# Kernel tuning notes

Hardware: AMD Instinct MI355X
Metric: run time of the kernel (lower is better)

The kernel has to match this reference:

```python
import jax, jax.numpy as jnp
import numpy as np

T_MAX = 20
NUM_HEADS = 8
COMPLEXITY_W = 0.3
LN_EPS = 1e-5


def _layernorm(h, g, b):
    mu = jnp.mean(h, axis=-1, keepdims=True)
    var = jnp.var(h, axis=-1, keepdims=True)
    return (h - mu) / jnp.sqrt(var + LN_EPS) * g + b


def _gate_mlp(x, W1, b1, g, be, W2, b2, W3, b3):
    # Linear -> LayerNorm -> ReLU -> (Dropout=id in eval) -> Linear -> ReLU -> Linear -> Sigmoid
    h = jax.nn.relu(_layernorm(x @ W1 + b1, g, be))
    h = jax.nn.relu(h @ W2 + b2)
    return jax.nn.sigmoid(h @ W3 + b3)


def _adaptive_windows(x, p):
    S = x.shape[1]
    gate = _gate_mlp(x, p['gW1'], p['gb1'], p['gg'], p['gbe'], p['gW2'], p['gb2'], p['gW3'], p['gb3'])
    comp = _gate_mlp(x, p['cW1'], p['cb1'], p['cg'], p['cbe'], p['cW2'], p['cb2'], p['cW3'], p['cb3'])
    pos = jnp.linspace(0.8, 1.2, S, dtype=x.dtype).reshape(1, -1, 1)
    score = ((1.0 - COMPLEXITY_W) * gate + COMPLEXITY_W * comp) * pos
    T_i = jnp.clip(jnp.ceil(score[..., 0] * T_MAX), 1, T_MAX).astype(jnp.int32)  # [B,S]
    return T_i


def _spike_sum(x, T_i, alpha, beta):
    # LIF recurrence over T_MAX steps; accumulate masked spikes. x: [B,S,E]
    z = jnp.zeros_like(x)

    def step(carry, t):
        v, i, acc = carry
        active = (t < T_i).astype(x.dtype)[..., None]  # [B,S,1]
        i = alpha * i + x * active
        v = beta * v + i
        s = (v >= 1.0).astype(x.dtype)
        v = v * (1.0 - s)  # v_reset = 0
        return (v, i, acc + s * active), None

    (_, _, acc), _ = jax.lax.scan(step, (z, z, z), jnp.arange(T_MAX))
    return acc


def _forward(x, params):
    B, S, E = x.shape
    H, D = NUM_HEADS, E // NUM_HEADS
    q = x @ params['Wq']
    k = x @ params['Wk']
    v = x @ params['Wv']
    T_i = _adaptive_windows(x, params)
    q_sum = _spike_sum(q, T_i, params['alpha_q'], params['beta_q'])
    k_sum = _spike_sum(k, T_i, params['alpha_k'], params['beta_k'])
    v_mean = _spike_sum(v, T_i, params['alpha_v'], params['beta_v']) / T_MAX
    q_sum = q_sum.reshape(B, S, H, D)
    k_sum = k_sum.reshape(B, S, H, D)
    v_mean = v_mean.reshape(B, S, H, D)
    scale = D ** -0.5
    scores = jnp.einsum('bihd,bjhd->bhij', q_sum, k_sum) * scale
    w = jax.nn.softmax(scores, axis=-1)
    out = jnp.einsum('bhij,bjhd->bihd', w, v_mean).reshape(B, S, E)
    return out @ params['Wo'] + params['bo']


def setup_inputs() -> dict:
    key = jax.random.key(0)
    ks = iter(jax.random.split(key, 32))
    B, S, E = 4, 1024, 512
    f32 = jnp.float32

    def w(shape, scale=0.02):
        return jax.random.normal(next(ks), shape, dtype=f32) * scale

    inp = {
        'x': jax.random.normal(next(ks), (B, S, E), dtype=f32),
        'Wq': w((E, E)), 'Wk': w((E, E)), 'Wv': w((E, E)),
        'Wo': w((E, E)), 'bo': jnp.zeros((E,), f32),
        'gW1': w((E, 128)), 'gb1': jnp.zeros((128,), f32),
        'gg': jnp.ones((128,), f32), 'gbe': jnp.zeros((128,), f32),
        'gW2': w((128, 64)), 'gb2': jnp.zeros((64,), f32),
        'gW3': w((64, 1)), 'gb3': jnp.zeros((1,), f32),
        'cW1': w((E, 64)), 'cb1': jnp.zeros((64,), f32),
        'cg': jnp.ones((64,), f32), 'cbe': jnp.zeros((64,), f32),
        'cW2': w((64, 32)), 'cb2': jnp.zeros((32,), f32),
        'cW3': w((32, 1)), 'cb3': jnp.zeros((1,), f32),
        'alpha_q': jnp.asarray(np.exp(-1 / 5.0), f32), 'beta_q': jnp.asarray(np.exp(-1 / 20.0), f32),
        'alpha_k': jnp.asarray(np.exp(-1 / 5.0), f32), 'beta_k': jnp.asarray(np.exp(-1 / 20.0), f32),
        'alpha_v': jnp.asarray(np.exp(-1 / 5.0), f32), 'beta_v': jnp.asarray(np.exp(-1 / 20.0), f32),
    }
    return inp


def reference(x, Wq, Wk, Wv, Wo, bo,
              gW1, gb1, gg, gbe, gW2, gb2, gW3, gb3,
              cW1, cb1, cg, cbe, cW2, cb2, cW3, cb3,
              alpha_q, beta_q, alpha_k, beta_k, alpha_v, beta_v):
    params = dict(Wq=Wq, Wk=Wk, Wv=Wv, Wo=Wo, bo=bo,
                  gW1=gW1, gb1=gb1, gg=gg, gbe=gbe, gW2=gW2, gb2=gb2, gW3=gW3, gb3=gb3,
                  cW1=cW1, cb1=cb1, cg=cg, cbe=cbe, cW2=cW2, cb2=cb2, cW3=cW3, cb3=cb3,
                  alpha_q=alpha_q, beta_q=beta_q, alpha_k=alpha_k, beta_k=beta_k,
                  alpha_v=alpha_v, beta_v=beta_v)
    return _forward(x, params)
```

## Files before the change

kernel.cpp:

```cpp
#include <hip/hip_runtime.h>
#include <math.h>

#define SEQ   1024
#define EMB   512
#define NROWS 4096
#define LDP   72
#define GROWS 4

typedef __attribute__((ext_vector_type(8))) short short8;
typedef __attribute__((ext_vector_type(4))) float float4v;

__device__ __forceinline__ float bf2f(unsigned short s) {
    union { float f; unsigned u; } x; x.u = ((unsigned)s) << 16; return x.f;
}
__device__ __forceinline__ unsigned short f2bf(float f) {
    union { float f; unsigned u; } x; x.f = f;
    unsigned r = x.u + 0x7fffu + ((x.u >> 16) & 1u);
    return (unsigned short)(r >> 16);
}

__device__ __forceinline__ void gld16(const unsigned short* g, short* l) {
    __builtin_amdgcn_global_load_lds(
        (__attribute__((address_space(1))) void*)(g),
        (__attribute__((address_space(3))) void*)(l), 16, 0, 0);
}

__device__ __forceinline__ void split3(float x, unsigned short& h, unsigned short& m, unsigned short& l) {
    union { float f; unsigned u; } a; a.f = x;
    const unsigned rh = a.u + 0x7fffu + ((a.u >> 16) & 1u);
    h = (unsigned short)(rh >> 16);
    union { float f; unsigned u; } hf; hf.u = rh & 0xffff0000u;
    const float r1 = x - hf.f;
    a.f = r1;
    const unsigned rm = a.u + 0x7fffu + ((a.u >> 16) & 1u);
    m = (unsigned short)(rm >> 16);
    union { float f; unsigned u; } mf; mf.u = rm & 0xffff0000u;
    const float r2 = r1 - mf.f;
    l = f2bf(r2);
}

template<int H1, int H2>
__device__ __forceinline__ double mlp_eval(
    const double xs[GROWS][EMB], double* h1, double* h2, double* red,
    double* mu_s, double* var_s,
    const float* __restrict__ W1, const float* __restrict__ b1,
    const float* __restrict__ gam, const float* __restrict__ bet,
    const float* __restrict__ W2, const float* __restrict__ b2,
    const float* __restrict__ W3, const float* __restrict__ b3,
    int tid, int myrow)
{
    constexpr int S  = 256 / H1;
    constexpr int KS = EMB / S;

    {
        const int col = tid % H1, sk = tid / H1;
        double acc[GROWS] = {0.0, 0.0, 0.0, 0.0};
        const int kbeg = sk * KS;
        #pragma unroll 4
        for (int k = kbeg; k < kbeg + KS; ++k) {
            const double w = (double)W1[k * H1 + col];
            #pragma unroll
            for (int r = 0; r < GROWS; ++r) acc[r] += w * xs[r][k];
        }
        #pragma unroll
        for (int r = 0; r < GROWS; ++r) red[(sk * GROWS + r) * H1 + col] = acc[r];
    }
    __syncthreads();
    for (int idx = tid; idx < GROWS * H1; idx += 256) {
        const int r = idx / H1, cc = idx % H1;
        double s = 0.0;
        #pragma unroll
        for (int t = 0; t < S; ++t) s += red[(t * GROWS + r) * H1 + cc];
        h1[r * H1 + cc] = s + (double)b1[cc];
    }
    __syncthreads();

    {
        const int w = tid >> 6, l = tid & 63;
        double s = 0.0;
        for (int c = l; c < H1; c += 64) s += h1[w * H1 + c];
        #pragma unroll
        for (int off = 32; off >= 1; off >>= 1) s += __shfl_xor(s, off);
        if (l == 0) mu_s[w] = s / (double)H1;
    }
    __syncthreads();
    {
        const int w = tid >> 6, l = tid & 63;
        const double mu = mu_s[w];
        double s = 0.0;
        for (int c = l; c < H1; c += 64) { const double d = h1[w * H1 + c] - mu; s += d * d; }
        #pragma unroll
        for (int off = 32; off >= 1; off >>= 1) s += __shfl_xor(s, off);
        if (l == 0) var_s[w] = s / (double)H1;
    }
    __syncthreads();
    for (int idx = tid; idx < GROWS * H1; idx += 256) {
        const int r = idx / H1, cc = idx % H1;
        double hn = (h1[r * H1 + cc] - mu_s[r]) / sqrt(var_s[r] + 1e-5) * (double)gam[cc] + (double)bet[cc];
        h1[r * H1 + cc] = hn > 0.0 ? hn : 0.0;
    }
    __syncthreads();

    {
        const int col = tid % H2;
        const int r   = tid / H2;
        if (r < GROWS) {
            double acc = (double)b2[col];
            for (int k = 0; k < H1; ++k)
                acc += (double)W2[k * H2 + col] * h1[r * H1 + k];
            h2[r * H2 + col] = acc > 0.0 ? acc : 0.0;
        }
    }
    __syncthreads();

    {
        const int w = tid >> 6, l = tid & 63;
        double s = 0.0;
        for (int c = l; c < H2; c += 64) s += h2[w * H2 + c] * (double)W3[c];
        #pragma unroll
        for (int off = 32; off >= 1; off >>= 1) s += __shfl_xor(s, off);
        if (l == 0) mu_s[w] = s;
    }
    __syncthreads();
    double ret = 0.0;
    if (myrow >= 0) {
        const double z = mu_s[myrow] + (double)b3[0];
        ret = 1.0 / (1.0 + exp(-z));
    }
    return ret;
}

__global__ __launch_bounds__(256) void pre_kernel(
    const float* __restrict__ x,
    const float* __restrict__ gW1, const float* __restrict__ gb1,
    const float* __restrict__ gg,  const float* __restrict__ gbe,
    const float* __restrict__ gW2, const float* __restrict__ gb2,
    const float* __restrict__ gW3, const float* __restrict__ gb3,
    const float* __restrict__ cW1, const float* __restrict__ cb1,
    const float* __restrict__ cg,  const float* __restrict__ cbe,
    const float* __restrict__ cW2, const float* __restrict__ cb2,
    const float* __restrict__ cW3, const float* __restrict__ cb3,
    double* __restrict__ scores,
    const float* __restrict__ Wq, const float* __restrict__ Wk,
    const float* __restrict__ Wv, unsigned short* __restrict__ WL,
    unsigned short* __restrict__ XL,
    const float* __restrict__ Wo, unsigned short* __restrict__ WoT)
{
    __shared__ __align__(16) char smem[30784];
    const int bid = blockIdx.x;
    const int tid = threadIdx.x;

    if (bid < 2048) {
        double (*xs)[EMB] = (double(*)[EMB])smem;
        double* h1    = (double*)(smem + 16384);
        double* h2    = (double*)(smem + 20480);
        double* red   = (double*)(smem + 22528);
        double* mu_s  = (double*)(smem + 30720);
        double* var_s = (double*)(smem + 30752);

        const int gx = bid & 1023, gy = bid >> 10;
        const int row0 = gx * GROWS;

        for (int idx = tid; idx < GROWS * EMB; idx += 256) {
            const int r = idx >> 9, cc = idx & 511;
            xs[r][cc] = (double)x[(size_t)(row0 + r) * EMB + cc];
        }
        __syncthreads();

        const int myrow = (tid < GROWS) ? tid : -1;
        double v;
        if (gy == 0)
            v = mlp_eval<128, 64>(xs, h1, h2, red, mu_s, var_s,
                                  gW1, gb1, gg, gbe, gW2, gb2, gW3, gb3, tid, myrow);
        else
            v = mlp_eval<64, 32>(xs, h1, h2, red, mu_s, var_s,
                                 cW1, cb1, cg, cbe, cW2, cb2, cW3, cb3, tid, myrow);

        if (myrow >= 0)
            scores[(size_t)gy * NROWS + row0 + myrow] = v;

    } else if (bid < 3072) {
        unsigned short* Xh = XL;
        unsigned short* Xm = XL + (size_t)NROWS * EMB;
        unsigned short* Xl = Xm + (size_t)NROWS * EMB;
        const size_t i0 = ((size_t)(bid - 2048) * 256 + tid) * 8;
        const float4 a0 = *(const float4*)&x[i0];
        const float4 a1 = *(const float4*)&x[i0 + 4];
        const float av8[8] = {a0.x, a0.y, a0.z, a0.w, a1.x, a1.y, a1.z, a1.w};
        short8 ph, pm, pl;
        #pragma unroll
        for (int e = 0; e < 8; ++e) {
            unsigned short h, m, l;
            split3(av8[e], h, m, l);
            ph[e] = (short)h; pm[e] = (short)m; pl[e] = (short)l;
        }
        *(short8*)&Xh[i0] = ph;
        *(short8*)&Xm[i0] = pm;
        *(short8*)&Xl[i0] = pl;

    } else if (bid < 3264) {
        const int t = bid - 3072;
        const int z = t >> 6, rem = t & 63;
        const int k0 = (rem >> 3) * 64, n0 = (rem & 7) * 64;
        const float* __restrict__ W = (z == 0) ? Wq : (z == 1) ? Wk : Wv;
        unsigned short* Th = WL + (size_t)z * 3 * EMB * EMB;
        unsigned short* Tm = Th + (size_t)EMB * EMB;
        unsigned short* Tl = Tm + (size_t)EMB * EMB;

        float (*Ws)[68] = (float(*)[68])smem;
        #pragma unroll
        for (int it = 0; it < 4; ++it) {
            const int idx = it * 256 + tid;
            const int r = idx >> 4, c4 = (idx & 15) * 4;
            *(float4*)&Ws[r][c4] = *(const float4*)&W[(size_t)(k0 + r) * EMB + n0 + c4];
        }
        __syncthreads();
        #pragma unroll
        for (int it = 0; it < 2; ++it) {
            const int idx = it * 256 + tid;
            const int n = idx >> 3, k8 = (idx & 7) * 8;
            short8 ph, pm, pl;
            #pragma unroll
            for (int j = 0; j < 8; ++j) {
                unsigned short h, m, l;
                split3(Ws[k8 + j][n], h, m, l);
                ph[j] = (short)h; pm[j] = (short)m; pl[j] = (short)l;
            }
            const size_t o = (size_t)(n0 + n) * EMB + k0 + k8;
            *(short8*)&Th[o] = ph;
            *(short8*)&Tm[o] = pm;
            *(short8*)&Tl[o] = pl;
        }

    } else {
        const int t = bid - 3264;
        const int k0 = (t >> 3) * 64, n0 = (t & 7) * 64;
        unsigned short (*Ws)[72] = (unsigned short(*)[72])smem;
        #pragma unroll
        for (int it = 0; it < 4; ++it) {
            const int idx = it * 256 + tid;
            const int r = idx >> 4, c4 = (idx & 15) * 4;
            const float4 w4 = *(const float4*)&Wo[(size_t)(k0 + r) * EMB + n0 + c4];
            Ws[r][c4 + 0] = f2bf(w4.x); Ws[r][c4 + 1] = f2bf(w4.y);
            Ws[r][c4 + 2] = f2bf(w4.z); Ws[r][c4 + 3] = f2bf(w4.w);
        }
        __syncthreads();
        #pragma unroll
        for (int it = 0; it < 2; ++it) {
            const int idx = it * 256 + tid;
            const int n = idx >> 3, k8 = (idx & 7) * 8;
            short8 pack;
            #pragma unroll
            for (int j = 0; j < 8; ++j) pack[j] = (short)Ws[k8 + j][n];
            *(short8*)&WoT[(size_t)(n0 + n) * EMB + k0 + k8] = pack;
        }
    }
}

__global__ __launch_bounds__(256) void qkv_mfma_lif_kernel(
    const unsigned short* __restrict__ XL, const unsigned short* __restrict__ WL,
    const float* __restrict__ aq, const float* __restrict__ bq,
    const float* __restrict__ akp, const float* __restrict__ bkp,
    const float* __restrict__ av, const float* __restrict__ bv,
    const double* __restrict__ scores,
    unsigned short* __restrict__ q_sum, unsigned short* __restrict__ k_sum,
    unsigned short* __restrict__ v_mean)
{
    const int z = blockIdx.z;
    const unsigned short* __restrict__ WTh = WL + (size_t)z * 3 * EMB * EMB;
    const unsigned short* __restrict__ WTm = WTh + (size_t)EMB * EMB;
    const unsigned short* __restrict__ WTl = WTm + (size_t)EMB * EMB;
    const unsigned short* __restrict__ Xh = XL;
    const unsigned short* __restrict__ Xm = XL + (size_t)NROWS * EMB;
    const unsigned short* __restrict__ Xl = Xm + (size_t)NROWS * EMB;
    unsigned short* __restrict__ out = (z == 0) ? q_sum : (z == 1) ? k_sum : v_mean;
    const double alpha = (double)((z == 0) ? aq : (z == 1) ? akp : av)[0];
    const double beta  = (double)((z == 0) ? bq : (z == 1) ? bkp : bv)[0];

    const int phys = blockIdx.x + 8 * blockIdx.y;
    const int logical = (phys & 7) * 32 + (phys >> 3);
    const int bx = logical & 7, by = logical >> 3;
    const int row0 = by * 128, col0 = bx * 64;

    __shared__ __align__(16) short As[3][4096];
    __shared__ __align__(16) short Bs[3][2048];

    const int tid  = threadIdx.x;
    const int lane = tid & 63, wave = tid >> 6;
    const int qd = lane >> 4, c = lane & 15;
    const int wrow = wave * 32;

    const int kc8 = ((lane & 3) ^ ((lane >> 3) & 3)) * 8;
    const size_t ga0 = (size_t)(row0 + wave * 16 + (lane >> 2)) * EMB + kc8;
    const size_t ga1 = ga0 + (size_t)64 * EMB;
    const size_t gb  = (size_t)(col0 + wave * 16 + (lane >> 2)) * EMB + kc8;

    int arf[2], brf[4];
    #pragma unroll
    for (int i = 0; i < 2; ++i) {
        const int Ra = wrow + i * 16 + c;
        arf[i] = Ra * 32 + ((qd ^ ((Ra >> 1) & 3)) * 8);
    }
    #pragma unroll
    for (int j = 0; j < 4; ++j) {
        const int Rb = j * 16 + c;
        brf[j] = Rb * 32 + ((qd ^ ((Rb >> 1) & 3)) * 8);
    }

    float4v acc[2][4];
    #pragma unroll
    for (int i = 0; i < 2; ++i)
        #pragma unroll
        for (int j = 0; j < 4; ++j)
            acc[i][j] = (float4v){0.f, 0.f, 0.f, 0.f};

    for (int k0 = 0; k0 < EMB; k0 += 32) {
        __syncthreads();
        gld16(Xh  + ga0 + k0, &As[0][wave * 512]);
        gld16(Xh  + ga1 + k0, &As[0][2048 + wave * 512]);
        gld16(Xm  + ga0 + k0, &As[1][wave * 512]);
        gld16(Xm  + ga1 + k0, &As[1][2048 + wave * 512]);
        gld16(Xl  + ga0 + k0, &As[2][wave * 512]);
        gld16(Xl  + ga1 + k0, &As[2][2048 + wave * 512]);
        gld16(WTh + gb  + k0, &Bs[0][wave * 512]);
        gld16(WTm + gb  + k0, &Bs[1][wave * 512]);
        gld16(WTl + gb  + k0, &Bs[2][wave * 512]);
        __syncthreads();

        short8 Afh[2], Afm[2], Afl[2];
        #pragma unroll
        for (int i = 0; i < 2; ++i) {
            Afh[i] = *(const short8*)&As[0][arf[i]];
            Afm[i] = *(const short8*)&As[1][arf[i]];
            Afl[i] = *(const short8*)&As[2][arf[i]];
        }
        short8 Bfh[4], Bfm[4], Bfl[4];
        #pragma unroll
        for (int j = 0; j < 4; ++j) {
            Bfh[j] = *(const short8*)&Bs[0][brf[j]];
            Bfm[j] = *(const short8*)&Bs[1][brf[j]];
            Bfl[j] = *(const short8*)&Bs[2][brf[j]];
        }

        #pragma unroll
        for (int i = 0; i < 2; ++i)
            #pragma unroll
            for (int j = 0; j < 4; ++j) {
                float4v t = acc[i][j];
                t = __builtin_amdgcn_mfma_f32_16x16x32_bf16(Afh[i], Bfh[j], t, 0, 0, 0);
                t = __builtin_amdgcn_mfma_f32_16x16x32_bf16(Afh[i], Bfm[j], t, 0, 0, 0);
                t = __builtin_amdgcn_mfma_f32_16x16x32_bf16(Afm[i], Bfh[j], t, 0, 0, 0);
                t = __builtin_amdgcn_mfma_f32_16x16x32_bf16(Afm[i], Bfm[j], t, 0, 0, 0);
                t = __builtin_amdgcn_mfma_f32_16x16x32_bf16(Afh[i], Bfl[j], t, 0, 0, 0);
                t = __builtin_amdgcn_mfma_f32_16x16x32_bf16(Afl[i], Bfh[j], t, 0, 0, 0);
                acc[i][j] = t;
            }
    }

    #pragma unroll
    for (int i = 0; i < 2; ++i)
        #pragma unroll
        for (int r = 0; r < 4; ++r) {
            const int gm = row0 + wrow + i * 16 + qd * 4 + r;
            const double g0 = scores[gm];
            const double c0 = scores[NROWS + gm];
            const int s = gm & (SEQ - 1);
            const double step = (1.2 - 0.8) / (double)(SEQ - 1);
            const double pos  = (double)s * step + 0.8;
            const double score = ((1.0 - 0.3) * g0 + 0.3 * c0) * pos;
            double td = ceil(score * 20.0);
            td = td < 1.0 ? 1.0 : (td > 20.0 ? 20.0 : td);
            const int T = (int)td;
            double cur0 = 0.0, cur1 = 0.0, cur2 = 0.0, cur3 = 0.0;
            double vm0 = 0.0, vm1 = 0.0, vm2 = 0.0, vm3 = 0.0;
            double sp0 = 0.0, sp1 = 0.0, sp2 = 0.0, sp3 = 0.0;
            const double xv0 = (double)acc[i][0][r];
            const double xv1 = (double)acc[i][1][r];
            const double xv2 = (double)acc[i][2][r];
            const double xv3 = (double)acc[i][3][r];
            for (int t = 0; t < T; ++t) {
                cur0 = alpha * cur0 + xv0; vm0 = beta * vm0 + cur0;
                if (vm0 >= 1.0) { sp0 += 1.0; vm0 = 0.0; }
                cur1 = alpha * cur1 + xv1; vm1 = beta * vm1 + cur1;
                if (vm1 >= 1.0) { sp1 += 1.0; vm1 = 0.0; }
                cur2 = alpha * cur2 + xv2; vm2 = beta * vm2 + cur2;
                if (vm2 >= 1.0) { sp2 += 1.0; vm2 = 0.0; }
                cur3 = alpha * cur3 + xv3; vm3 = beta * vm3 + cur3;
                if (vm3 >= 1.0) { sp3 += 1.0; vm3 = 0.0; }
            }
            if (z == 2) { sp0 /= 20.0; sp1 /= 20.0; sp2 /= 20.0; sp3 /= 20.0; }
            const size_t ob = (size_t)gm * EMB + col0 + c;
            out[ob +  0] = f2bf((float)sp0);
            out[ob + 16] = f2bf((float)sp1);
            out[ob + 32] = f2bf((float)sp2);
            out[ob + 48] = f2bf((float)sp3);
        }
}

__global__ __launch_bounds__(256) void attn_mfma_kernel(
    const unsigned short* __restrict__ q, const unsigned short* __restrict__ k,
    const unsigned short* __restrict__ v, unsigned short* __restrict__ attn_bf)
{
    __shared__ __align__(16) short Ks[64 * LDP];
    __shared__ __align__(16) short Pt[64 * LDP];
    __shared__ __align__(16) short Vt[64 * LDP];

    const int b = blockIdx.z, h = blockIdx.y;
    const int i0 = blockIdx.x * 64;
    const int tid  = threadIdx.x;
    const int wave = tid >> 6, lane = tid & 63;
    const int quad = lane >> 4, c = lane & 15;

    const unsigned short* Qb = q + ((size_t)b * SEQ + i0) * EMB + h * 64;
    const unsigned short* Kb = k + (size_t)b * SEQ * EMB + h * 64;
    const unsigned short* Vb = v + (size_t)b * SEQ * EMB + h * 64;

    short8 qf[2];
    {
        const int qrow = wave * 16 + c;
        #pragma unroll
        for (int ks = 0; ks < 2; ++ks) {
            short8 raw = *(const short8*)(Qb + (size_t)qrow * EMB + ks * 32 + quad * 8);
            short8 sc8;
            #pragma unroll
            for (int j = 0; j < 8; ++j)
                sc8[j] = (short)f2bf(bf2f((unsigned short)raw[j]) * 0.125f);
            qf[ks] = sc8;
        }
    }

    float m_r[4], l_r[4];
    float4v o[4];
    #pragma unroll
    for (int r = 0; r < 4; ++r) { m_r[r] = -1e30f; l_r[r] = 0.f; }
    #pragma unroll
    for (int nb = 0; nb < 4; ++nb)
        #pragma unroll
        for (int r = 0; r < 4; ++r) o[nb][r] = 0.f;

    for (int jt = 0; jt < SEQ / 64; ++jt) {
        #pragma unroll
        for (int it = 0; it < 2; ++it) {
            const int idx = it * 256 + tid;
            const int row = idx >> 3, ch = idx & 7;
            short8 val = *(const short8*)(Kb + (size_t)(jt * 64 + row) * EMB + ch * 8);
            *(short8*)&Ks[row * LDP + ch * 8] = val;
        }
        __syncthreads();

        float sc[4][4];
        #pragma unroll
        for (int nb = 0; nb < 4; ++nb) {
            float4v acc = {0.f, 0.f, 0.f, 0.f};
            #pragma unroll
            for (int ks = 0; ks < 2; ++ks) {
                short8 bfrag = *(const short8*)&Ks[(nb * 16 + c) * LDP + ks * 32 + quad * 8];
                acc = __builtin_amdgcn_mfma_f32_16x16x32_bf16(qf[ks], bfrag, acc, 0, 0, 0);
            }
            #pragma unroll
            for (int r = 0; r < 4; ++r) sc[nb][r] = acc[r];
        }

        float mnew[4], alpha[4];
        #pragma unroll
        for (int r = 0; r < 4; ++r) {
            float mx = fmaxf(fmaxf(sc[0][r], sc[1][r]), fmaxf(sc[2][r], sc[3][r]));
            #pragma unroll
            for (int off = 8; off >= 1; off >>= 1) mx = fmaxf(mx, __shfl_xor(mx, off));
            mnew[r]  = fmaxf(m_r[r], mx);
            alpha[r] = __expf(m_r[r] - mnew[r]);
            m_r[r]   = mnew[r];
        }
        float psum[4] = {0.f, 0.f, 0.f, 0.f};
        #pragma unroll
        for (int nb = 0; nb < 4; ++nb)
            #pragma unroll
            for (int r = 0; r < 4; ++r) {
                float p = __expf(sc[nb][r] - mnew[r]);
                psum[r] += p;
                Pt[(wave * 16 + quad * 4 + r) * LDP + nb * 16 + c] = (short)f2bf(p);
            }
        #pragma unroll
        for (int r = 0; r < 4; ++r) {
            float s = psum[r];
            #pragma unroll
            for (int off = 8; off >= 1; off >>= 1) s += __shfl_xor(s, off);
            l_r[r] = l_r[r] * alpha[r] + s;
            #pragma unroll
            for (int nb = 0; nb < 4; ++nb) o[nb][r] *= alpha[r];
        }

        {
            const int m = tid & 7, rp = tid >> 3;
            const int r = rp * 2;
            short8 v0 = *(const short8*)(Vb + (size_t)(jt * 64 + r) * EMB + m * 8);
            short8 v1 = *(const short8*)(Vb + (size_t)(jt * 64 + r + 1) * EMB + m * 8);
            const int rch = r >> 3, rlow = r & 7;
            #pragma unroll
            for (int i = 0; i < 8; ++i) {
                const int d = m * 8 + i;
                const int col = ((rch ^ m) << 3) + rlow;
                *(int*)&Vt[d * LDP + col] =
                    (int)((unsigned)(unsigned short)v0[i] |
                          ((unsigned)(unsigned short)v1[i] << 16));
            }
        }
        __syncthreads();

        short8 pf[2];
        #pragma unroll
        for (int ks = 0; ks < 2; ++ks)
            pf[ks] = *(const short8*)&Pt[(wave * 16 + c) * LDP + ks * 32 + quad * 8];
        #pragma unroll
        for (int nb = 0; nb < 4; ++nb) {
            float4v acc = o[nb];
            #pragma unroll
            for (int ks = 0; ks < 2; ++ks) {
                const int d = nb * 16 + c;
                const int kch = ks * 4 + quad;
                const int col = ((kch ^ (d >> 3)) << 3);
                short8 vfrag = *(const short8*)&Vt[d * LDP + col];
                acc = __builtin_amdgcn_mfma_f32_16x16x32_bf16(pf[ks], vfrag, acc, 0, 0, 0);
            }
            o[nb] = acc;
        }
    }

    #pragma unroll
    for (int r = 0; r < 4; ++r) {
        const float inv = 1.0f / l_r[r];
        const int row = i0 + wave * 16 + quad * 4 + r;
        #pragma unroll
        for (int nb = 0; nb < 4; ++nb)
            attn_bf[((size_t)b * SEQ + row) * EMB + h * 64 + nb * 16 + c] =
                f2bf(o[nb][r] * inv);
    }
}

__global__ __launch_bounds__(256) void out_gemm_kernel(
    const unsigned short* __restrict__ A,
    const unsigned short* __restrict__ BT,
    const float* __restrict__ bias, float* __restrict__ out)
{
    __shared__ __align__(16) short Ao[2048], Bo[2048];

    const int tid  = threadIdx.x;
    const int lane = tid & 63, wave = tid >> 6;
    const int qd = lane >> 4, c = lane & 15;

    const int phys = blockIdx.x + 8 * blockIdx.y;
    const int logical = (phys & 7) * 64 + (phys >> 3);
    const int bx = logical & 7, by = logical >> 3;
    const int row0 = by * 64, col0 = bx * 64;

    const int kc8 = ((lane & 3) ^ ((lane >> 3) & 3)) * 8;
    const size_t ga = (size_t)(row0 + wave * 16 + (lane >> 2)) * EMB + kc8;
    const size_t gb = (size_t)(col0 + wave * 16 + (lane >> 2)) * EMB + kc8;

    int arf, brf[4];
    {
        const int Ra = wave * 16 + c;
        arf = Ra * 32 + ((qd ^ ((Ra >> 1) & 3)) * 8);
    }
    #pragma unroll
    for (int j = 0; j < 4; ++j) {
        const int Rb = j * 16 + c;
        brf[j] = Rb * 32 + ((qd ^ ((Rb >> 1) & 3)) * 8);
    }

    float4v acc[4];
    #pragma unroll
    for (int j = 0; j < 4; ++j) acc[j] = (float4v){0.f, 0.f, 0.f, 0.f};

    for (int k0 = 0; k0 < EMB; k0 += 32) {
        __syncthreads();
        gld16(A  + ga + k0, &Ao[wave * 512]);
        gld16(BT + gb + k0, &Bo[wave * 512]);
        __syncthreads();

        const short8 af = *(const short8*)&Ao[arf];
        #pragma unroll
        for (int j = 0; j < 4; ++j) {
            const short8 bf = *(const short8*)&Bo[brf[j]];
            acc[j] = __builtin_amdgcn_mfma_f32_16x16x32_bf16(af, bf, acc[j], 0, 0, 0);
        }
    }

    #pragma unroll
    for (int j = 0; j < 4; ++j)
        #pragma unroll
        for (int r = 0; r < 4; ++r) {
            const int gm = row0 + wave * 16 + qd * 4 + r;
            const int gn = col0 + j * 16 + c;
            out[(size_t)gm * EMB + gn] = acc[j][r] + bias[gn];
        }
}

extern "C" void kernel_launch(void* const* d_in, const int* in_sizes, int n_in,
                              void* d_out, int out_size, void* d_ws, size_t ws_size,
                              hipStream_t stream)
{
    const float* x   = (const float*)d_in[0];
    const float* Wq  = (const float*)d_in[1];
    const float* Wk  = (const float*)d_in[2];
    const float* Wv  = (const float*)d_in[3];
    const float* Wo  = (const float*)d_in[4];
    const float* bo  = (const float*)d_in[5];
    const float* gW1 = (const float*)d_in[6];
    const float* gb1 = (const float*)d_in[7];
    const float* gg  = (const float*)d_in[8];
    const float* gbe = (const float*)d_in[9];
    const float* gW2 = (const float*)d_in[10];
    const float* gb2 = (const float*)d_in[11];
    const float* gW3 = (const float*)d_in[12];
    const float* gb3 = (const float*)d_in[13];
    const float* cW1 = (const float*)d_in[14];
    const float* cb1 = (const float*)d_in[15];
    const float* cg  = (const float*)d_in[16];
    const float* cbe = (const float*)d_in[17];
    const float* cW2 = (const float*)d_in[18];
    const float* cb2 = (const float*)d_in[19];
    const float* cW3 = (const float*)d_in[20];
    const float* cb3 = (const float*)d_in[21];
    const float* aq  = (const float*)d_in[22];
    const float* bq  = (const float*)d_in[23];
    const float* ak  = (const float*)d_in[24];
    const float* bk  = (const float*)d_in[25];
    const float* av  = (const float*)d_in[26];
    const float* bv  = (const float*)d_in[27];

    unsigned short* q_sum   = (unsigned short*)((char*)d_ws + 16384);
    unsigned short* k_sum   = q_sum   + (size_t)NROWS * EMB;
    unsigned short* v_mean  = k_sum   + (size_t)NROWS * EMB;
    unsigned short* attn_bf = v_mean  + (size_t)NROWS * EMB;
    unsigned short* WoT     = attn_bf + (size_t)NROWS * EMB;
    unsigned short* WL      = WoT     + (size_t)EMB * EMB;
    unsigned short* XLp     = WL      + (size_t)9 * EMB * EMB;
    double* scores          = (double*)(XLp + (size_t)3 * NROWS * EMB);
    float* out = (float*)d_out;

    pre_kernel<<<dim3(3328), dim3(256), 0, stream>>>(
        x, gW1, gb1, gg, gbe, gW2, gb2, gW3, gb3,
        cW1, cb1, cg, cbe, cW2, cb2, cW3, cb3, scores,
        Wq, Wk, Wv, WL, XLp, Wo, WoT);

    qkv_mfma_lif_kernel<<<dim3(EMB / 64, NROWS / 128, 3), dim3(256), 0, stream>>>(
        XLp, WL, aq, bq, ak, bk, av, bv, scores, q_sum, k_sum, v_mean);

    attn_mfma_kernel<<<dim3(SEQ / 64, 8, 4), dim3(256), 0, stream>>>(
        q_sum, k_sum, v_mean, attn_bf);

    out_gemm_kernel<<<dim3(EMB / 64, NROWS / 64), dim3(256), 0, stream>>>(
        attn_bf, WoT, bo, out);
}
```

Before: 250.9 us.

## Double-buffer K/V tiles in attention and A/B tiles in output GEMM

The attention kernel now prefetches the next K and V tiles into registers while it computes the current tile, then stores them into a second LDS buffer. This removes one __syncthreads per iteration and hides global load latency. The output GEMM likewise switches from direct global-to-LDS loads with a K-step of 32 to register-prefetched, double-buffered 64-wide K tiles with a new XOR swizzle. The trade-off is more LDS and more registers per block, which may lower occupancy.

```diff
diff --git a/kernel.cpp b/kernel.cpp
--- a/kernel.cpp
+++ b/kernel.cpp
@@ -401,9 +401,9 @@
     const unsigned short* __restrict__ q, const unsigned short* __restrict__ k,
     const unsigned short* __restrict__ v, unsigned short* __restrict__ attn_bf)
 {
-    __shared__ __align__(16) short Ks[64 * LDP];
+    __shared__ __align__(16) short Ks2[2][64 * LDP];
+    __shared__ __align__(16) short Vt2[2][64 * LDP];
     __shared__ __align__(16) short Pt[64 * LDP];
-    __shared__ __align__(16) short Vt[64 * LDP];
 
     const int b = blockIdx.z, h = blockIdx.y;
     const int i0 = blockIdx.x * 64;
@@ -429,6 +429,29 @@
         }
     }
 
+    const int krow = tid >> 3, kch = tid & 7;
+    const int vm_  = tid & 7,  vrp = tid >> 3;
+    const int vr   = vrp * 2;
+    const int vrch = vr >> 3, vrlow = vr & 7;
+
+    short8 kr0, kr1, vv0, vv1;
+    kr0 = *(const short8*)(Kb + (size_t)krow * EMB + kch * 8);
+    kr1 = *(const short8*)(Kb + (size_t)(32 + krow) * EMB + kch * 8);
+    vv0 = *(const short8*)(Vb + (size_t)vr * EMB + vm_ * 8);
+    vv1 = *(const short8*)(Vb + (size_t)(vr + 1) * EMB + vm_ * 8);
+    {
+        *(short8*)&Ks2[0][krow * LDP + kch * 8] = kr0;
+        *(short8*)&Ks2[0][(32 + krow) * LDP + kch * 8] = kr1;
+        #pragma unroll
+        for (int i = 0; i < 8; ++i) {
+            const int d = vm_ * 8 + i;
+            const int col = ((vrch ^ vm_) << 3) + vrlow;
+            *(int*)&Vt2[0][d * LDP + col] =
+                (int)((unsigned)(unsigned short)vv0[i] |
+                      ((unsigned)(unsigned short)vv1[i] << 16));
+        }
+    }
+
     float m_r[4], l_r[4];
     float4v o[4];
     #pragma unroll
@@ -439,14 +462,17 @@
         for (int r = 0; r < 4; ++r) o[nb][r] = 0.f;
 
     for (int jt = 0; jt < SEQ / 64; ++jt) {
-        #pragma unroll
-        for (int it = 0; it < 2; ++it) {
-            const int idx = it * 256 + tid;
-            const int row = idx >> 3, ch = idx & 7;
-            short8 val = *(const short8*)(Kb + (size_t)(jt * 64 + row) * EMB + ch * 8);
-            *(short8*)&Ks[row * LDP + ch * 8] = val;
-        }
         __syncthreads();
+        const short* Ks = &Ks2[jt & 1][0];
+        const short* Vt = &Vt2[jt & 1][0];
+
+        if (jt + 1 < SEQ / 64) {
+            const size_t kb = (size_t)((jt + 1) * 64);
+            kr0 = *(const short8*)(Kb + (kb + krow) * EMB + kch * 8);
+            kr1 = *(const short8*)(Kb + (kb + 32 + krow) * EMB + kch * 8);
+            vv0 = *(const short8*)(Vb + (kb + vr) * EMB + vm_ * 8);
+            vv1 = *(const short8*)(Vb + (kb + vr + 1) * EMB + vm_ * 8);
+        }
 
         float sc[4][4];
         #pragma unroll
@@ -490,23 +516,6 @@
             for (int nb = 0; nb < 4; ++nb) o[nb][r] *= alpha[r];
         }
 
-        {
-            const int m = tid & 7, rp = tid >> 3;
-            const int r = rp * 2;
-            short8 v0 = *(const short8*)(Vb + (size_t)(jt * 64 + r) * EMB + m * 8);
-            short8 v1 = *(const short8*)(Vb + (size_t)(jt * 64 + r + 1) * EMB + m * 8);
-            const int rch = r >> 3, rlow = r & 7;
-            #pragma unroll
-            for (int i = 0; i < 8; ++i) {
-                const int d = m * 8 + i;
-                const int col = ((rch ^ m) << 3) + rlow;
-                *(int*)&Vt[d * LDP + col] =
-                    (int)((unsigned)(unsigned short)v0[i] |
-                          ((unsigned)(unsigned short)v1[i] << 16));
-            }
-        }
-        __syncthreads();
-
         short8 pf[2];
         #pragma unroll
         for (int ks = 0; ks < 2; ++ks)
@@ -517,12 +526,26 @@
             #pragma unroll
             for (int ks = 0; ks < 2; ++ks) {
                 const int d = nb * 16 + c;
-                const int kch = ks * 4 + quad;
-                const int col = ((kch ^ (d >> 3)) << 3);
+                const int kch2 = ks * 4 + quad;
+                const int col = ((kch2 ^ (d >> 3)) << 3);
                 short8 vfrag = *(const short8*)&Vt[d * LDP + col];
                 acc = __builtin_amdgcn_mfma_f32_16x16x32_bf16(pf[ks], vfrag, acc, 0, 0, 0);
             }
             o[nb] = acc;
+        }
+
+        if (jt + 1 < SEQ / 64) {
+            const int nb2 = (jt + 1) & 1;
+            *(short8*)&Ks2[nb2][krow * LDP + kch * 8] = kr0;
+            *(short8*)&Ks2[nb2][(32 + krow) * LDP + kch * 8] = kr1;
+            #pragma unroll
+            for (int i = 0; i < 8; ++i) {
+                const int d = vm_ * 8 + i;
+                const int col = ((vrch ^ vm_) << 3) + vrlow;
+                *(int*)&Vt2[nb2][d * LDP + col] =
+                    (int)((unsigned)(unsigned short)vv0[i] |
+                          ((unsigned)(unsigned short)vv1[i] << 16));
+            }
         }
     }
 
@@ -542,7 +565,7 @@
     const unsigned short* __restrict__ BT,
     const float* __restrict__ bias, float* __restrict__ out)
 {
-    __shared__ __align__(16) short Ao[2048], Bo[2048];
+    __shared__ __align__(16) short As2[2][4096], Bs2[2][4096];
 
     const int tid  = threadIdx.x;
     const int lane = tid & 63, wave = tid >> 6;
@@ -553,36 +576,52 @@
     const int bx = logical & 7, by = logical >> 3;
     const int row0 = by * 64, col0 = bx * 64;
 
-    const int kc8 = ((lane & 3) ^ ((lane >> 3) & 3)) * 8;
-    const size_t ga = (size_t)(row0 + wave * 16 + (lane >> 2)) * EMB + kc8;
-    const size_t gb = (size_t)(col0 + wave * 16 + (lane >> 2)) * EMB + kc8;
-
-    int arf, brf[4];
-    {
-        const int Ra = wave * 16 + c;
-        arf = Ra * 32 + ((qd ^ ((Ra >> 1) & 3)) * 8);
-    }
-    #pragma unroll
-    for (int j = 0; j < 4; ++j) {
-        const int Rb = j * 16 + c;
-        brf[j] = Rb * 32 + ((qd ^ ((Rb >> 1) & 3)) * 8);
+    const int sr = tid >> 2, sj = (tid & 3) * 2;
+    const size_t gA = (size_t)(row0 + sr) * EMB + sj * 8;
+    const size_t gB = (size_t)(col0 + sr) * EMB + sj * 8;
+    const int dA0 = sr * 64 + ((sj ^ (sr & 7)) * 8);
+    const int dA1 = sr * 64 + (((sj + 1) ^ (sr & 7)) * 8);
+
+    int arf[2], brf[4][2];
+    #pragma unroll
+    for (int kk = 0; kk < 2; ++kk) {
+        arf[kk] = (wave * 16 + c) * 64 + (((kk * 4 + qd) ^ (c & 7)) * 8);
+        #pragma unroll
+        for (int j = 0; j < 4; ++j)
+            brf[j][kk] = (j * 16 + c) * 64 + (((kk * 4 + qd) ^ (c & 7)) * 8);
     }
 
     float4v acc[4];
     #pragma unroll
     for (int j = 0; j < 4; ++j) acc[j] = (float4v){0.f, 0.f, 0.f, 0.f};
 
-    for (int k0 = 0; k0 < EMB; k0 += 32) {
+    short8 ra0, ra1, rb0, rb1;
+    ra0 = *(const short8*)&A[gA];      ra1 = *(const short8*)&A[gA + 8];
+    rb0 = *(const short8*)&BT[gB];     rb1 = *(const short8*)&BT[gB + 8];
+    *(short8*)&As2[0][dA0] = ra0; *(short8*)&As2[0][dA1] = ra1;
+    *(short8*)&Bs2[0][dA0] = rb0; *(short8*)&Bs2[0][dA1] = rb1;
+
+    for (int it = 0; it < 8; ++it) {
         __syncthreads();
-        gld16(A  + ga + k0, &Ao[wave * 512]);
-        gld16(BT + gb + k0, &Bo[wave * 512]);
-        __syncthreads();
-
-        const short8 af = *(const short8*)&Ao[arf];
-        #pragma unroll
-        for (int j = 0; j < 4; ++j) {
-            const short8 bf = *(const short8*)&Bo[brf[j]];
-            acc[j] = __builtin_amdgcn_mfma_f32_16x16x32_bf16(af, bf, acc[j], 0, 0, 0);
+        const int cur = it & 1;
+        if (it < 7) {
+            const int k0 = (it + 1) * 64;
+            ra0 = *(const short8*)&A[gA + k0];  ra1 = *(const short8*)&A[gA + k0 + 8];
+            rb0 = *(const short8*)&BT[gB + k0]; rb1 = *(const short8*)&BT[gB + k0 + 8];
+        }
+        #pragma unroll
+        for (int kk = 0; kk < 2; ++kk) {
+            const short8 af = *(const short8*)&As2[cur][arf[kk]];
+            #pragma unroll
+            for (int j = 0; j < 4; ++j) {
+                const short8 bf = *(const short8*)&Bs2[cur][brf[j][kk]];
+                acc[j] = __builtin_amdgcn_mfma_f32_16x16x32_bf16(af, bf, acc[j], 0, 0, 0);
+            }
+        }
+        if (it < 7) {
+            const int nxt = cur ^ 1;
+            *(short8*)&As2[nxt][dA0] = ra0; *(short8*)&As2[nxt][dA1] = ra1;
+            *(short8*)&Bs2[nxt][dA0] = rb0; *(short8*)&Bs2[nxt][dA1] = rb1;
         }
     }
 
```

After: 248.3 us, median of 2. Within noise of the previous version (-1.1%).

## Split attention KV range across two blocks with combine pass; double-buffer out GEMM

Applied to the files above, without the earlier changes.

The attention kernel now splits the key/value sequence into two halves and launches twice as many blocks. Each block writes unnormalized fp32 partial outputs plus its running max and sum to workspace, and a new combine kernel merges them flash-decoding style into bf16. This targets low occupancy on the attention launch (512 blocks on a large GPU), at the cost of extra fp32 traffic and an extra launch. Separately, the output GEMM moves to 64-wide K tiles with register-staged double buffering in swizzled LDS, halving the barriers and overlapping global loads with MFMA work.

```diff
diff --git a/kernel.cpp b/kernel.cpp
--- a/kernel.cpp
+++ b/kernel.cpp
@@ -399,13 +399,15 @@
 
 __global__ __launch_bounds__(256) void attn_mfma_kernel(
     const unsigned short* __restrict__ q, const unsigned short* __restrict__ k,
-    const unsigned short* __restrict__ v, unsigned short* __restrict__ attn_bf)
+    const unsigned short* __restrict__ v,
+    float* __restrict__ OP, float* __restrict__ MP, float* __restrict__ LP)
 {
     __shared__ __align__(16) short Ks[64 * LDP];
     __shared__ __align__(16) short Pt[64 * LDP];
     __shared__ __align__(16) short Vt[64 * LDP];
 
-    const int b = blockIdx.z, h = blockIdx.y;
+    const int b = blockIdx.z & 3, kv = blockIdx.z >> 2;
+    const int h = blockIdx.y;
     const int i0 = blockIdx.x * 64;
     const int tid  = threadIdx.x;
     const int wave = tid >> 6, lane = tid & 63;
@@ -438,7 +440,7 @@
         #pragma unroll
         for (int r = 0; r < 4; ++r) o[nb][r] = 0.f;
 
-    for (int jt = 0; jt < SEQ / 64; ++jt) {
+    for (int jt = kv * 8; jt < kv * 8 + 8; ++jt) {
         #pragma unroll
         for (int it = 0; it < 2; ++it) {
             const int idx = it * 256 + tid;
@@ -526,15 +528,43 @@
         }
     }
 
+    const size_t grb = (size_t)(b * 8 + h) * SEQ;
     #pragma unroll
     for (int r = 0; r < 4; ++r) {
-        const float inv = 1.0f / l_r[r];
         const int row = i0 + wave * 16 + quad * 4 + r;
+        const size_t gr = grb + row;
+        float* op = OP + (size_t)kv * 32768 * 64 + gr * 64;
         #pragma unroll
         for (int nb = 0; nb < 4; ++nb)
-            attn_bf[((size_t)b * SEQ + row) * EMB + h * 64 + nb * 16 + c] =
-                f2bf(o[nb][r] * inv);
-    }
+            op[nb * 16 + c] = o[nb][r];
+        if (c == 0) {
+            MP[(size_t)kv * 32768 + gr] = m_r[r];
+            LP[(size_t)kv * 32768 + gr] = l_r[r];
+        }
+    }
+}
+
+__global__ __launch_bounds__(256) void attn_combine_kernel(
+    const float* __restrict__ OP, const float* __restrict__ MP,
+    const float* __restrict__ LP, unsigned short* __restrict__ attn_bf)
+{
+    const int idx = blockIdx.x * 256 + threadIdx.x;
+    const int gr = idx >> 3;
+    const int c8 = (idx & 7) * 8;
+    const float m0 = MP[gr], m1 = MP[32768 + gr];
+    const float l0 = LP[gr], l1 = LP[32768 + gr];
+    const float m  = fmaxf(m0, m1);
+    const float a0 = __expf(m0 - m), a1 = __expf(m1 - m);
+    const float inv = 1.0f / (l0 * a0 + l1 * a1);
+    const int bh = gr >> 10, row = gr & (SEQ - 1);
+    const int b = bh >> 3, h = bh & 7;
+    const float* p0 = OP + (size_t)gr * 64 + c8;
+    const float* p1 = OP + (size_t)32768 * 64 + (size_t)gr * 64 + c8;
+    short8 pack;
+    #pragma unroll
+    for (int j = 0; j < 8; ++j)
+        pack[j] = (short)f2bf((p0[j] * a0 + p1[j] * a1) * inv);
+    *(short8*)&attn_bf[((size_t)b * SEQ + row) * EMB + h * 64 + c8] = pack;
 }
 
 __global__ __launch_bounds__(256) void out_gemm_kernel(
@@ -542,7 +572,7 @@
     const unsigned short* __restrict__ BT,
     const float* __restrict__ bias, float* __restrict__ out)
 {
-    __shared__ __align__(16) short Ao[2048], Bo[2048];
+    __shared__ __align__(16) short As2[2][4096], Bs2[2][4096];
 
     const int tid  = threadIdx.x;
     const int lane = tid & 63, wave = tid >> 6;
@@ -553,36 +583,52 @@
     const int bx = logical & 7, by = logical >> 3;
     const int row0 = by * 64, col0 = bx * 64;
 
-    const int kc8 = ((lane & 3) ^ ((lane >> 3) & 3)) * 8;
-    const size_t ga = (size_t)(row0 + wave * 16 + (lane >> 2)) * EMB + kc8;
-    const size_t gb = (size_t)(col0 + wave * 16 + (lane >> 2)) * EMB + kc8;
-
-    int arf, brf[4];
-    {
-        const int Ra = wave * 16 + c;
-        arf = Ra * 32 + ((qd ^ ((Ra >> 1) & 3)) * 8);
-    }
-    #pragma unroll
-    for (int j = 0; j < 4; ++j) {
-        const int Rb = j * 16 + c;
-        brf[j] = Rb * 32 + ((qd ^ ((Rb >> 1) & 3)) * 8);
+    const int sr = tid >> 2, sj = (tid & 3) * 2;
+    const size_t gA = (size_t)(row0 + sr) * EMB + sj * 8;
+    const size_t gB = (size_t)(col0 + sr) * EMB + sj * 8;
+    const int dA0 = sr * 64 + ((sj ^ (sr & 7)) * 8);
+    const int dA1 = sr * 64 + (((sj + 1) ^ (sr & 7)) * 8);
+
+    int arf[2], brf[4][2];
+    #pragma unroll
+    for (int kk = 0; kk < 2; ++kk) {
+        arf[kk] = (wave * 16 + c) * 64 + (((kk * 4 + qd) ^ (c & 7)) * 8);
+        #pragma unroll
+        for (int j = 0; j < 4; ++j)
+            brf[j][kk] = (j * 16 + c) * 64 + (((kk * 4 + qd) ^ (c & 7)) * 8);
     }
 
     float4v acc[4];
     #pragma unroll
     for (int j = 0; j < 4; ++j) acc[j] = (float4v){0.f, 0.f, 0.f, 0.f};
 
-    for (int k0 = 0; k0 < EMB; k0 += 32) {
+    short8 ra0, ra1, rb0, rb1;
+    ra0 = *(const short8*)&A[gA];      ra1 = *(const short8*)&A[gA + 8];
+    rb0 = *(const short8*)&BT[gB];     rb1 = *(const short8*)&BT[gB + 8];
+    *(short8*)&As2[0][dA0] = ra0; *(short8*)&As2[0][dA1] = ra1;
+    *(short8*)&Bs2[0][dA0] = rb0; *(short8*)&Bs2[0][dA1] = rb1;
+
+    for (int it = 0; it < 8; ++it) {
         __syncthreads();
-        gld16(A  + ga + k0, &Ao[wave * 512]);
-        gld16(BT + gb + k0, &Bo[wave * 512]);
-        __syncthreads();
-
-        const short8 af = *(const short8*)&Ao[arf];
-        #pragma unroll
-        for (int j = 0; j < 4; ++j) {
-            const short8 bf = *(const short8*)&Bo[brf[j]];
-            acc[j] = __builtin_amdgcn_mfma_f32_16x16x32_bf16(af, bf, acc[j], 0, 0, 0);
+        const int cur = it & 1;
+        if (it < 7) {
+            const int k0 = (it + 1) * 64;
+            ra0 = *(const short8*)&A[gA + k0];  ra1 = *(const short8*)&A[gA + k0 + 8];
+            rb0 = *(const short8*)&BT[gB + k0]; rb1 = *(const short8*)&BT[gB + k0 + 8];
+        }
+        #pragma unroll
+        for (int kk = 0; kk < 2; ++kk) {
+            const short8 af = *(const short8*)&As2[cur][arf[kk]];
+            #pragma unroll
+            for (int j = 0; j < 4; ++j) {
+                const short8 bf = *(const short8*)&Bs2[cur][brf[j][kk]];
+                acc[j] = __builtin_amdgcn_mfma_f32_16x16x32_bf16(af, bf, acc[j], 0, 0, 0);
+            }
+        }
+        if (it < 7) {
+            const int nxt = cur ^ 1;
+            *(short8*)&As2[nxt][dA0] = ra0; *(short8*)&As2[nxt][dA1] = ra1;
+            *(short8*)&Bs2[nxt][dA0] = rb0; *(short8*)&Bs2[nxt][dA1] = rb1;
         }
     }
 
@@ -637,6 +683,9 @@
     unsigned short* WL      = WoT     + (size_t)EMB * EMB;
     unsigned short* XLp     = WL      + (size_t)9 * EMB * EMB;
     double* scores          = (double*)(XLp + (size_t)3 * NROWS * EMB);
+    float* OP               = (float*)(scores + 2 * NROWS);
+    float* MP               = OP + (size_t)2 * 32768 * 64;
+    float* LP               = MP + (size_t)2 * 32768;
     float* out = (float*)d_out;
 
     pre_kernel<<<dim3(3328), dim3(256), 0, stream>>>(
@@ -647,8 +696,11 @@
     qkv_mfma_lif_kernel<<<dim3(EMB / 64, NROWS / 128, 3), dim3(256), 0, stream>>>(
         XLp, WL, aq, bq, ak, bk, av, bv, scores, q_sum, k_sum, v_mean);
 
-    attn_mfma_kernel<<<dim3(SEQ / 64, 8, 4), dim3(256), 0, stream>>>(
-        q_sum, k_sum, v_mean, attn_bf);
+    attn_mfma_kernel<<<dim3(SEQ / 64, 8, 8), dim3(256), 0, stream>>>(
+        q_sum, k_sum, v_mean, OP, MP, LP);
+
+    attn_combine_kernel<<<dim3(1024), dim3(256), 0, stream>>>(
+        OP, MP, LP, attn_bf);
 
     out_gemm_kernel<<<dim3(EMB / 64, NROWS / 64), dim3(256), 0, stream>>>(
         attn_bf, WoT, bo, out);
```

Measured after the change: 253.4 us. Within noise of the previous version (+1.0%).
